# Kernel tuning notes

Measured on AMD Instinct MI355X. Metric: run time of the kernel, lower is better.

The kernel has to match this reference:

```python
import jax, jax.numpy as jnp
import numpy as np

N, D_IN, D_OUT = 4096, 1024, 1024


def setup_inputs() -> dict:
    key = jax.random.key(0)
    kx, kq, kk, kv = jax.random.split(key, 4)
    s = 1.0 / np.sqrt(D_IN)
    return {
        "x": jax.random.normal(kx, (N, D_IN), dtype=jnp.float32),
        "Wq": jax.random.normal(kq, (D_OUT, D_IN), dtype=jnp.float32) * s,
        "Wk": jax.random.normal(kk, (D_OUT, D_IN), dtype=jnp.float32) * s,
        "Wv": jax.random.normal(kv, (D_OUT, D_IN), dtype=jnp.float32) * s,
    }


def reference(x, Wq, Wk, Wv):
    # nn.Linear(d_in, d_out, bias=False): y = x @ W.T with W: [d_out, d_in]
    q = x @ Wq.T            # [N, d_out]
    k = x @ Wk.T            # [N, d_out]
    v = x @ Wv.T            # [N, d_out]
    scores = q @ k.T        # [N, N]
    scale = 1.0 / jnp.sqrt(jnp.asarray(k.shape[-1], dtype=x.dtype))
    attn = jax.nn.softmax(scores * scale, axis=-1)
    return attn @ v         # [N, d_out]
```

## Files before the change

### kernel.cpp

```cpp
#include <hip/hip_runtime.h>


typedef __attribute__((ext_vector_type(8))) __bf16 bf16x8;
typedef __attribute__((ext_vector_type(4))) float floatx4;

#define GLB_AS __attribute__((address_space(1)))
#define LDS_AS __attribute__((address_space(3)))

static __device__ __forceinline__ unsigned short f2bf_u16(float f) {
  union { float f; unsigned u; } x; x.f = f;
  unsigned r = x.u;
  r += 0x7fffu + ((r >> 16) & 1u);
  return (unsigned short)(r >> 16);
}

__global__ __launch_bounds__(256) void cast_f32_bf16(const float* __restrict__ in,
                                                     unsigned short* __restrict__ out) {
  int i = blockIdx.x * 256 + threadIdx.x;
  float4 v = reinterpret_cast<const float4*>(in)[i];
  ushort4 o = make_ushort4(f2bf_u16(v.x), f2bf_u16(v.y), f2bf_u16(v.z), f2bf_u16(v.w));
  reinterpret_cast<ushort4*>(out)[i] = o;
}

__global__ __launch_bounds__(256) void transpose_bf16(const unsigned short* __restrict__ in, int inLd,
                                                      unsigned short* __restrict__ out, int outLd) {
  __shared__ unsigned short tl[32][33];
  const int bi = blockIdx.y, bj = blockIdx.x;
  const int tx = threadIdx.x & 31, ty = threadIdx.x >> 5;
#pragma unroll
  for (int p = 0; p < 4; ++p)
    tl[ty + p * 8][tx] = in[(size_t)(bi * 32 + ty + p * 8) * inLd + bj * 32 + tx];
  __syncthreads();
#pragma unroll
  for (int p = 0; p < 4; ++p)
    out[(size_t)(bj * 32 + ty + p * 8) * outLd + bi * 32 + tx] = tl[tx][ty + p * 8];
}

struct GemmOuts { void* c[4]; int ldc[4]; };

template <int EPI>
__global__ __launch_bounds__(512, 2) void gemm256(const unsigned short* __restrict__ A,
                                                  const unsigned short* __restrict__ B,
                                                  GemmOuts outs, int lda, int ldb,
                                                  int klen, float scale) {
  __shared__ unsigned short sh[65536];
  const int t = threadIdx.x;
  const int w = t >> 6, lane = t & 63;
  const int wm = w >> 2, wn = w & 3;
  const int row0 = blockIdx.y * 256;
  const int col0 = blockIdx.x * 256;
  const int z = blockIdx.z;
  const int kstart = z * klen;
  const int NT = klen >> 5;

  const int sr  = t >> 2;
  const int scb = ((t & 3) * 16) ^ (((t >> 3) & 3) << 4);
  const unsigned short* gA0 = A + (size_t)(row0 + sr) * lda + kstart + (scb >> 1);
  const unsigned short* gA1 = gA0 + (size_t)128 * lda;
  const unsigned short* gB0 = B + (size_t)(col0 + sr) * ldb + kstart + (scb >> 1);
  const unsigned short* gB1 = gB0 + (size_t)128 * ldb;

#define STAGE_A(tl_) { const int b_ = (tl_) & 3; \
    __builtin_amdgcn_global_load_lds((const GLB_AS void*)(gA0 + (tl_) * 32), \
        (LDS_AS void*)&sh[b_ * 16384 + (w << 9)], 16, 0, 0); \
    __builtin_amdgcn_global_load_lds((const GLB_AS void*)(gA1 + (tl_) * 32), \
        (LDS_AS void*)&sh[b_ * 16384 + 4096 + (w << 9)], 16, 0, 0); }
#define STAGE_B(tl_) { const int b_ = (tl_) & 3; \
    __builtin_amdgcn_global_load_lds((const GLB_AS void*)(gB0 + (tl_) * 32), \
        (LDS_AS void*)&sh[b_ * 16384 + 8192 + (w << 9)], 16, 0, 0); \
    __builtin_amdgcn_global_load_lds((const GLB_AS void*)(gB1 + (tl_) * 32), \
        (LDS_AS void*)&sh[b_ * 16384 + 12288 + (w << 9)], 16, 0, 0); }

  const int fr = lane & 15;
  const int fc = (lane >> 4) * 16;
  int aoff[8], boff[4];
#pragma unroll
  for (int mf = 0; mf < 8; ++mf) {
    int off = ((wm * 128 + mf * 16 + fr) << 6) + fc;
    off ^= ((off >> 7) & 3) << 4;
    aoff[mf] = off >> 1;
  }
#pragma unroll
  for (int nf = 0; nf < 4; ++nf) {
    int off = ((wn * 64 + nf * 16 + fr) << 6) + fc;
    off ^= ((off >> 7) & 3) << 4;
    boff[nf] = off >> 1;
  }

  floatx4 acc[8][4] = {};

  STAGE_A(0) STAGE_B(0) STAGE_A(1) STAGE_B(1) STAGE_A(2) STAGE_B(2)
  asm volatile("s_waitcnt vmcnt(8)" ::: "memory");
  __builtin_amdgcn_s_barrier();

  for (int tile = 0; tile < NT; ++tile) {
    if (tile + 3 < NT) { STAGE_A(tile + 3) STAGE_B(tile + 3) }

    const int ab = (tile & 3) * 16384;
    const int bb = ab + 8192;
    bf16x8 af[8], bf[4];
#pragma unroll
    for (int mf = 0; mf < 8; ++mf) af[mf] = *(const bf16x8*)&sh[ab + aoff[mf]];
#pragma unroll
    for (int nf = 0; nf < 4; ++nf) bf[nf] = *(const bf16x8*)&sh[bb + boff[nf]];

    __builtin_amdgcn_s_setprio(1);
#pragma unroll
    for (int mf = 0; mf < 8; ++mf)
#pragma unroll
      for (int nf = 0; nf < 4; ++nf)
        acc[mf][nf] = __builtin_amdgcn_mfma_f32_16x16x32_bf16(af[mf], bf[nf], acc[mf][nf], 0, 0, 0);
    __builtin_amdgcn_s_setprio(0);

    if (tile <= NT - 4)      { asm volatile("s_waitcnt vmcnt(8)" ::: "memory"); }
    else if (tile == NT - 3) { asm volatile("s_waitcnt vmcnt(4)" ::: "memory"); }
    else if (tile == NT - 2) { asm volatile("s_waitcnt vmcnt(0)" ::: "memory"); }
    __builtin_amdgcn_s_barrier();
  }

#undef STAGE_A
#undef STAGE_B

  float* Cf = (float*)outs.c[z];
  unsigned short* Cb = (unsigned short*)outs.c[z];
  const int ldc = outs.ldc[z];
  const int er = (lane >> 4) * 4;
  const int ec = lane & 15;
#pragma unroll
  for (int mf = 0; mf < 8; ++mf)
#pragma unroll
    for (int nf = 0; nf < 4; ++nf)
#pragma unroll
      for (int r = 0; r < 4; ++r) {
        const int m = row0 + wm * 128 + mf * 16 + er + r;
        const int n = col0 + wn * 64 + nf * 16 + ec;
        const float v = acc[mf][nf][r] * scale;
        if (EPI == 0)      Cf[(size_t)m * ldc + n] = v;
        else if (EPI == 1) Cb[(size_t)m * ldc + n] = f2bf_u16(v);
        else               Cb[(size_t)m * ldc + n] = f2bf_u16(__expf(v));
      }
}

static __device__ __forceinline__ float bfpair(unsigned u) {
  union { unsigned u; float f; } a, b;
  a.u = u << 16; b.u = u & 0xffff0000u;
  return a.f + b.f;
}

__global__ __launch_bounds__(256) void rowsum_bf16(const unsigned short* __restrict__ P,
                                                   float* __restrict__ rs) {
  const int w = threadIdx.x >> 6, lane = threadIdx.x & 63;
  const int row = blockIdx.x * 4 + w;
  const uint4* p = (const uint4*)(P + (size_t)row * 4096);
  float s = 0.f;
#pragma unroll
  for (int c = 0; c < 8; ++c) {
    uint4 u = p[c * 64 + lane];
    s += bfpair(u.x) + bfpair(u.y) + bfpair(u.z) + bfpair(u.w);
  }
#pragma unroll
  for (int off = 32; off >= 1; off >>= 1) s += __shfl_xor(s, off);
  if (lane == 0) rs[row] = s;
}

__global__ __launch_bounds__(256) void reduce_pv(float* __restrict__ out,
                                                 const float* __restrict__ p1,
                                                 const float* __restrict__ p2,
                                                 const float* __restrict__ p3,
                                                 const float* __restrict__ rs) {
  const int row = blockIdx.x;
  const int idx = row * 256 + threadIdx.x;
  const float inv = 1.0f / rs[row];
  float4 o = ((const float4*)out)[idx];
  float4 a = ((const float4*)p1)[idx];
  float4 b = ((const float4*)p2)[idx];
  float4 c = ((const float4*)p3)[idx];
  o.x = (o.x + a.x + b.x + c.x) * inv;
  o.y = (o.y + a.y + b.y + c.y) * inv;
  o.z = (o.z + a.z + b.z + c.z) * inv;
  o.w = (o.w + a.w + b.w + c.w) * inv;
  ((float4*)out)[idx] = o;
}

extern "C" void kernel_launch(void* const* d_in, const int* in_sizes, int n_in,
                              void* d_out, int out_size, void* d_ws, size_t ws_size,
                              hipStream_t stream) {
  const float* x  = (const float*)d_in[0];
  const float* Wq = (const float*)d_in[1];
  const float* Wk = (const float*)d_in[2];
  const float* Wv = (const float*)d_in[3];
  float* out = (float*)d_out;

  const int N = 4096, D = 1024;

  char* ws = (char*)d_ws;
  unsigned short* P    = (unsigned short*)ws;
  float*          p1   = (float*)(ws + (32u << 20));
  float*          p2   = (float*)(ws + (48u << 20));
  unsigned short* xb   = (unsigned short*)(ws + (64u << 20));
  unsigned short* wb   = (unsigned short*)(ws + (72u << 20));
  unsigned short* qkvb = (unsigned short*)(ws + (78u << 20));
  float*          p3   = (float*)(ws + (78u << 20));
  float*          rs   = (float*)(ws + (94u << 20));
  unsigned short* vT   = xb;

  cast_f32_bf16<<<N * D / 1024, 256, 0, stream>>>(x, xb);
  cast_f32_bf16<<<D * D / 1024, 256, 0, stream>>>(Wq, wb);
  cast_f32_bf16<<<D * D / 1024, 256, 0, stream>>>(Wk, wb + (size_t)D * D);
  cast_f32_bf16<<<D * D / 1024, 256, 0, stream>>>(Wv, wb + (size_t)2 * D * D);

  GemmOuts oq; oq.c[0] = oq.c[1] = oq.c[2] = oq.c[3] = qkvb;
  oq.ldc[0] = oq.ldc[1] = oq.ldc[2] = oq.ldc[3] = 3 * D;
  gemm256<1><<<dim3(3 * D / 256, N / 256, 1), 512, 0, stream>>>(xb, wb, oq, D, D, D, 1.0f);

  transpose_bf16<<<dim3(D / 32, N / 32), 256, 0, stream>>>(qkvb + 2048, 3 * D, vT, N);

  GemmOuts os; os.c[0] = os.c[1] = os.c[2] = os.c[3] = P;
  os.ldc[0] = os.ldc[1] = os.ldc[2] = os.ldc[3] = N;
  gemm256<2><<<dim3(N / 256, N / 256, 1), 512, 0, stream>>>(qkvb, qkvb + D, os, 3 * D, 3 * D, D, 0.03125f);

  rowsum_bf16<<<N / 4, 256, 0, stream>>>(P, rs);

  GemmOuts op;
  op.c[0] = out; op.ldc[0] = D;
  op.c[1] = p1;  op.ldc[1] = D;
  op.c[2] = p2;  op.ldc[2] = D;
  op.c[3] = p3;  op.ldc[3] = D;
  gemm256<0><<<dim3(D / 256, N / 256, 4), 512, 0, stream>>>(P, vT, op, N, N, N / 4, 1.0f);

  reduce_pv<<<N, 256, 0, stream>>>(out, p1, p2, p3, rs);
}
```

Baseline: 160.7 us.

## Restructure GEMM main loop into BK=64 double-buffered tiles with interleaved sub-phases

The GEMM K-tile grows from 32 to 64 and the buffering drops from four stages to two, with each tile split into four half-phases. Each phase does its LDS fragment reads, issues one quarter-tile async global-to-LDS load, then runs an MFMA burst. Barriers, sched_barrier and a new XOR swizzle keep the phases ordered and avoid LDS bank conflicts. The aim is finer interleaving of memory traffic and matrix math and fewer loop iterations, at the cost of many more barriers per tile and a more fragile wait-count scheme.

Result: no change. 160.1 us (-0.4%).

```diff
diff --git a/kernel.cpp b/kernel.cpp
--- a/kernel.cpp
+++ b/kernel.cpp
@@ -51,75 +51,112 @@
   const int col0 = blockIdx.x * 256;
   const int z = blockIdx.z;
   const int kstart = z * klen;
-  const int NT = klen >> 5;
-
-  const int sr  = t >> 2;
-  const int scb = ((t & 3) * 16) ^ (((t >> 3) & 3) << 4);
-  const unsigned short* gA0 = A + (size_t)(row0 + sr) * lda + kstart + (scb >> 1);
+  const int NT = klen >> 6;
+
+  const int scbe = (((t & 3) ^ ((t >> 3) & 3)) << 3);
+  const unsigned short* gA0 = A + (size_t)(row0 + (t >> 2)) * lda + kstart + scbe;
   const unsigned short* gA1 = gA0 + (size_t)128 * lda;
-  const unsigned short* gB0 = B + (size_t)(col0 + sr) * ldb + kstart + (scb >> 1);
+  const unsigned short* gB0 = B + (size_t)(col0 + (t >> 2)) * ldb + kstart + scbe;
   const unsigned short* gB1 = gB0 + (size_t)128 * ldb;
 
-#define STAGE_A(tl_) { const int b_ = (tl_) & 3; \
-    __builtin_amdgcn_global_load_lds((const GLB_AS void*)(gA0 + (tl_) * 32), \
-        (LDS_AS void*)&sh[b_ * 16384 + (w << 9)], 16, 0, 0); \
-    __builtin_amdgcn_global_load_lds((const GLB_AS void*)(gA1 + (tl_) * 32), \
-        (LDS_AS void*)&sh[b_ * 16384 + 4096 + (w << 9)], 16, 0, 0); }
-#define STAGE_B(tl_) { const int b_ = (tl_) & 3; \
-    __builtin_amdgcn_global_load_lds((const GLB_AS void*)(gB0 + (tl_) * 32), \
-        (LDS_AS void*)&sh[b_ * 16384 + 8192 + (w << 9)], 16, 0, 0); \
-    __builtin_amdgcn_global_load_lds((const GLB_AS void*)(gB1 + (tl_) * 32), \
-        (LDS_AS void*)&sh[b_ * 16384 + 12288 + (w << 9)], 16, 0, 0); }
+#define STAGE_HALF(h_) do { \
+    const int tile_ = (h_) >> 2, opb_ = (h_) & 1, kh_ = ((h_) >> 1) & 1; \
+    const int lo_ = (((tile_) & 1) << 15) + (opb_ << 14) + (kh_ << 13) + (w << 9); \
+    const unsigned short* s0_ = (opb_ ? gB0 : gA0) + tile_ * 64 + kh_ * 32; \
+    const unsigned short* s1_ = (opb_ ? gB1 : gA1) + tile_ * 64 + kh_ * 32; \
+    __builtin_amdgcn_global_load_lds((const GLB_AS void*)s0_, (LDS_AS void*)&sh[lo_], 16, 0, 0); \
+    __builtin_amdgcn_global_load_lds((const GLB_AS void*)s1_, (LDS_AS void*)&sh[lo_ + 4096], 16, 0, 0); \
+  } while (0)
+#define STAGE_IF(h_) do { const int hh_ = (h_); if (hh_ < 4 * NT) STAGE_HALF(hh_); } while (0)
 
   const int fr = lane & 15;
-  const int fc = (lane >> 4) * 16;
-  int aoff[8], boff[4];
-#pragma unroll
-  for (int mf = 0; mf < 8; ++mf) {
-    int off = ((wm * 128 + mf * 16 + fr) << 6) + fc;
-    off ^= ((off >> 7) & 3) << 4;
-    aoff[mf] = off >> 1;
+  const int sg = (((lane >> 4) ^ ((lane >> 1) & 3)) << 3);
+  int aofs[8], bofs[4];
+#pragma unroll
+  for (int mf = 0; mf < 8; ++mf) aofs[mf] = ((wm * 128 + mf * 16 + fr) << 5) + sg;
+#pragma unroll
+  for (int nf = 0; nf < 4; ++nf) bofs[nf] = 16384 + ((wn * 64 + nf * 16 + fr) << 5) + sg;
+
+  floatx4 acc[8][4] = {};
+
+#pragma unroll
+  for (int h = 0; h < 7; ++h) STAGE_IF(h);
+  asm volatile("s_waitcnt vmcnt(6)" ::: "memory");
+  __builtin_amdgcn_s_barrier();
+
+  for (int tile = 0; tile < NT; ++tile) {
+    const int bo = (tile & 1) << 15;
+    bf16x8 a0[8], b0[2], b1[2];
+
+#pragma unroll
+    for (int mf = 0; mf < 8; ++mf) a0[mf] = *(const bf16x8*)&sh[bo + aofs[mf]];
+    b0[0] = *(const bf16x8*)&sh[bo + bofs[0]];
+    b0[1] = *(const bf16x8*)&sh[bo + bofs[1]];
+    STAGE_IF(4 * tile + 7);
+    __builtin_amdgcn_s_barrier();
+    asm volatile("s_waitcnt lgkmcnt(0)" ::: "memory");
+    __builtin_amdgcn_sched_barrier(0);
+    __builtin_amdgcn_s_setprio(1);
+#pragma unroll
+    for (int mf = 0; mf < 8; ++mf)
+#pragma unroll
+      for (int nf = 0; nf < 2; ++nf)
+        acc[mf][nf] = __builtin_amdgcn_mfma_f32_16x16x32_bf16(a0[mf], b0[nf], acc[mf][nf], 0, 0, 0);
+    __builtin_amdgcn_s_setprio(0);
+    __builtin_amdgcn_s_barrier();
+
+    b1[0] = *(const bf16x8*)&sh[bo + bofs[2]];
+    b1[1] = *(const bf16x8*)&sh[bo + bofs[3]];
+    STAGE_IF(4 * tile + 8);
+    __builtin_amdgcn_s_barrier();
+    asm volatile("s_waitcnt lgkmcnt(0)" ::: "memory");
+    __builtin_amdgcn_sched_barrier(0);
+    __builtin_amdgcn_s_setprio(1);
+#pragma unroll
+    for (int mf = 0; mf < 8; ++mf)
+#pragma unroll
+      for (int nf = 0; nf < 2; ++nf)
+        acc[mf][2 + nf] = __builtin_amdgcn_mfma_f32_16x16x32_bf16(a0[mf], b1[nf], acc[mf][2 + nf], 0, 0, 0);
+    __builtin_amdgcn_s_setprio(0);
+    __builtin_amdgcn_s_barrier();
+
+#pragma unroll
+    for (int mf = 0; mf < 8; ++mf) a0[mf] = *(const bf16x8*)&sh[bo + 8192 + aofs[mf]];
+    b0[0] = *(const bf16x8*)&sh[bo + 8192 + bofs[0]];
+    b0[1] = *(const bf16x8*)&sh[bo + 8192 + bofs[1]];
+    STAGE_IF(4 * tile + 9);
+    __builtin_amdgcn_s_barrier();
+    asm volatile("s_waitcnt lgkmcnt(0)" ::: "memory");
+    __builtin_amdgcn_sched_barrier(0);
+    __builtin_amdgcn_s_setprio(1);
+#pragma unroll
+    for (int mf = 0; mf < 8; ++mf)
+#pragma unroll
+      for (int nf = 0; nf < 2; ++nf)
+        acc[mf][nf] = __builtin_amdgcn_mfma_f32_16x16x32_bf16(a0[mf], b0[nf], acc[mf][nf], 0, 0, 0);
+    __builtin_amdgcn_s_setprio(0);
+    __builtin_amdgcn_s_barrier();
+
+    b1[0] = *(const bf16x8*)&sh[bo + 8192 + bofs[2]];
+    b1[1] = *(const bf16x8*)&sh[bo + 8192 + bofs[3]];
+    STAGE_IF(4 * tile + 10);
+    __builtin_amdgcn_s_barrier();
+    asm volatile("s_waitcnt lgkmcnt(0)" ::: "memory");
+    __builtin_amdgcn_sched_barrier(0);
+    __builtin_amdgcn_s_setprio(1);
+#pragma unroll
+    for (int mf = 0; mf < 8; ++mf)
+#pragma unroll
+      for (int nf = 0; nf < 2; ++nf)
+        acc[mf][2 + nf] = __builtin_amdgcn_mfma_f32_16x16x32_bf16(a0[mf], b1[nf], acc[mf][2 + nf], 0, 0, 0);
+    __builtin_amdgcn_s_setprio(0);
+    if (tile < NT - 2)       { asm volatile("s_waitcnt vmcnt(6)" ::: "memory"); }
+    else if (tile == NT - 2) { asm volatile("s_waitcnt vmcnt(0)" ::: "memory"); }
+    __builtin_amdgcn_s_barrier();
   }
-#pragma unroll
-  for (int nf = 0; nf < 4; ++nf) {
-    int off = ((wn * 64 + nf * 16 + fr) << 6) + fc;
-    off ^= ((off >> 7) & 3) << 4;
-    boff[nf] = off >> 1;
-  }
-
-  floatx4 acc[8][4] = {};
-
-  STAGE_A(0) STAGE_B(0) STAGE_A(1) STAGE_B(1) STAGE_A(2) STAGE_B(2)
-  asm volatile("s_waitcnt vmcnt(8)" ::: "memory");
-  __builtin_amdgcn_s_barrier();
-
-  for (int tile = 0; tile < NT; ++tile) {
-    if (tile + 3 < NT) { STAGE_A(tile + 3) STAGE_B(tile + 3) }
-
-    const int ab = (tile & 3) * 16384;
-    const int bb = ab + 8192;
-    bf16x8 af[8], bf[4];
-#pragma unroll
-    for (int mf = 0; mf < 8; ++mf) af[mf] = *(const bf16x8*)&sh[ab + aoff[mf]];
-#pragma unroll
-    for (int nf = 0; nf < 4; ++nf) bf[nf] = *(const bf16x8*)&sh[bb + boff[nf]];
-
-    __builtin_amdgcn_s_setprio(1);
-#pragma unroll
-    for (int mf = 0; mf < 8; ++mf)
-#pragma unroll
-      for (int nf = 0; nf < 4; ++nf)
-        acc[mf][nf] = __builtin_amdgcn_mfma_f32_16x16x32_bf16(af[mf], bf[nf], acc[mf][nf], 0, 0, 0);
-    __builtin_amdgcn_s_setprio(0);
-
-    if (tile <= NT - 4)      { asm volatile("s_waitcnt vmcnt(8)" ::: "memory"); }
-    else if (tile == NT - 3) { asm volatile("s_waitcnt vmcnt(4)" ::: "memory"); }
-    else if (tile == NT - 2) { asm volatile("s_waitcnt vmcnt(0)" ::: "memory"); }
-    __builtin_amdgcn_s_barrier();
-  }
-
-#undef STAGE_A
-#undef STAGE_B
+
+#undef STAGE_HALF
+#undef STAGE_IF
 
   float* Cf = (float*)outs.c[z];
   unsigned short* Cb = (unsigned short*)outs.c[z];
```
